# Kernel tuning notes

Measured on AMD Instinct MI355X. Metric: run time of the kernel, lower is better.

## Reference

```python
import jax, jax.numpy as jnp
import numpy as np

B, S, H, F, E, K = 4, 2048, 512, 2048, 8, 2


def setup_inputs() -> dict:
    key = jax.random.key(0)
    ks = jax.random.split(key, 6)
    s_h = 1.0 / np.sqrt(H)
    s_f = 1.0 / np.sqrt(F)
    return {
        "x": jax.random.normal(ks[0], (B, S, H), dtype=jnp.float32),
        "router_w": jax.random.uniform(ks[1], (E, H), jnp.float32, -s_h, s_h),
        "fc1_w": jax.random.uniform(ks[2], (E, F, H), jnp.float32, -s_h, s_h),
        "fc1_b": jax.random.uniform(ks[3], (E, F), jnp.float32, -s_h, s_h),
        "fc2_w": jax.random.uniform(ks[4], (E, H, F), jnp.float32, -s_f, s_f),
        "fc2_b": jax.random.uniform(ks[5], (E, H), jnp.float32, -s_f, s_f),
    }


def reference(x, router_w, fc1_w, fc1_b, fc2_w, fc2_b):
    # Router: Linear (no bias), softmax over experts, top-k, renormalize.
    logits = jnp.einsum("bsh,eh->bse", x, router_w)           # [B,S,E]
    probs = jax.nn.softmax(logits, axis=-1)                    # [B,S,E]
    topk_p, topk_i = jax.lax.top_k(probs, K)                   # [B,S,K]
    topk_p = topk_p / (jnp.sum(topk_p, axis=-1, keepdims=True) + 1e-9)

    # Original loop runs every expert FFN on all tokens and masks;
    # mathematically identical: dense per-expert FFN, then gather+combine.
    h1 = jnp.einsum("bsh,efh->bsef", x, fc1_w) + fc1_b         # [B,S,E,F]
    a = jax.nn.gelu(h1, approximate=False)                     # exact erf GELU (torch nn.GELU default)
    y = jnp.einsum("bsef,ehf->bseh", a, fc2_w) + fc2_b         # [B,S,E,H]

    sel = jnp.take_along_axis(y, topk_i[..., None], axis=2)    # [B,S,K,H]
    output = jnp.sum(topk_p[..., None] * sel, axis=2)          # [B,S,H]
    return output, probs, topk_i
```

## Files before the change

kernel.cpp:

```cpp
#include <hip/hip_runtime.h>

#define T_TOKENS 8192
#define HD 512
#define FD 2048
#define NE 8
#define CAP 8192
#define CSTRIDE 32

typedef __attribute__((ext_vector_type(8))) short short8;
typedef __attribute__((ext_vector_type(4))) float f32x4;

__device__ __forceinline__ ushort f2bf(float f) {
  union { float f; unsigned u; } v; v.f = f;
  unsigned u = v.u;
  return (ushort)((u + 0x7fffu + ((u >> 16) & 1u)) >> 16);
}

__device__ __forceinline__ void gld16(const ushort* g, ushort* l) {
  __builtin_amdgcn_global_load_lds(
      (const __attribute__((address_space(1))) void*)g,
      (__attribute__((address_space(3))) void*)l, 16, 0, 0);
}

__global__ void cvt_bf16_3(const float4* __restrict__ s0, ushort4* __restrict__ d0, int c0,
                           const float4* __restrict__ s1, ushort4* __restrict__ d1, int c1,
                           const float4* __restrict__ s2, ushort4* __restrict__ d2, int c2) {
  int i = blockIdx.x * blockDim.x + threadIdx.x;
  int st = gridDim.x * blockDim.x;
  int nt = c0 + c1 + c2;
  for (; i < nt; i += st) {
    const float4* s; ushort4* d; int j = i;
    if (j < c0) { s = s0; d = d0; }
    else if ((j -= c0) < c1) { s = s1; d = d1; }
    else { j -= c1; s = s2; d = d2; }
    float4 v = s[j];
    ushort4 o;
    o.x = f2bf(v.x); o.y = f2bf(v.y); o.z = f2bf(v.z); o.w = f2bf(v.w);
    d[j] = o;
  }
}

#define TPW 16
__global__ void router_kernel(const float* __restrict__ x, const float* __restrict__ rw,
                              float* __restrict__ probs_out, float* __restrict__ topk_out,
                              int* __restrict__ counts, int* __restrict__ bucket_tok,
                              float* __restrict__ bucket_w, int4* __restrict__ tok_info) {
  __shared__ int lcnt[NE];
  __shared__ int lbase[NE];
  __shared__ int ls_e0[64], ls_e1[64], ls_s0[64], ls_s1[64];
  __shared__ float ls_w0[64], ls_w1[64];

  int wave = threadIdx.x >> 6, lane = threadIdx.x & 63;
  if (threadIdx.x < NE) lcnt[threadIdx.x] = 0;
  __syncthreads();

  int tbase = blockIdx.x * 64;
  for (int it = 0; it < TPW; it++) {
    int lt = wave * TPW + it;
    int t = tbase + lt;
    float acc[NE];
#pragma unroll
    for (int e = 0; e < NE; e++) acc[e] = 0.f;
    const float* xr = x + (size_t)t * HD;
    for (int c = 0; c < HD; c += 64) {
      float xv = xr[c + lane];
#pragma unroll
      for (int e = 0; e < NE; e++) acc[e] += xv * rw[e * HD + c + lane];
    }
#pragma unroll
    for (int e = 0; e < NE; e++) {
#pragma unroll
      for (int s = 32; s > 0; s >>= 1) acc[e] += __shfl_xor(acc[e], s, 64);
    }
    if (lane == 0) {
      float m = acc[0];
#pragma unroll
      for (int e = 1; e < NE; e++) m = fmaxf(m, acc[e]);
      float p[NE], s = 0.f;
#pragma unroll
      for (int e = 0; e < NE; e++) { p[e] = expf(acc[e] - m); s += p[e]; }
      float inv = 1.f / s;
#pragma unroll
      for (int e = 0; e < NE; e++) { p[e] *= inv; probs_out[(size_t)t * NE + e] = p[e]; }
      int i0 = 0;
#pragma unroll
      for (int e = 1; e < NE; e++) if (p[e] > p[i0]) i0 = e;
      int i1 = (i0 == 0) ? 1 : 0;
#pragma unroll
      for (int e = 0; e < NE; e++) if (e != i0 && p[e] > p[i1]) i1 = e;
      float r = 1.f / (p[i0] + p[i1] + 1e-9f);
      topk_out[(size_t)t * 2 + 0] = (float)i0;
      topk_out[(size_t)t * 2 + 1] = (float)i1;
      ls_e0[lt] = i0; ls_e1[lt] = i1;
      ls_w0[lt] = p[i0] * r; ls_w1[lt] = p[i1] * r;
      ls_s0[lt] = atomicAdd(&lcnt[i0], 1);
      ls_s1[lt] = atomicAdd(&lcnt[i1], 1);
    }
  }
  __syncthreads();
  if (threadIdx.x < NE)
    lbase[threadIdx.x] = atomicAdd(&counts[threadIdx.x * CSTRIDE], lcnt[threadIdx.x]);
  __syncthreads();
  if (threadIdx.x < 64) {
    int lt = threadIdx.x, t = tbase + lt;
    int e0 = ls_e0[lt], e1 = ls_e1[lt];
    int g0 = lbase[e0] + ls_s0[lt];
    int g1 = lbase[e1] + ls_s1[lt];
    bucket_tok[e0 * CAP + g0] = t; bucket_w[e0 * CAP + g0] = ls_w0[lt];
    bucket_tok[e1 * CAP + g1] = t; bucket_w[e1 * CAP + g1] = ls_w1[lt];
    tok_info[t] = make_int4(e0, e1, g0, g1);
  }
}

__global__ void scan_kernel(const int* __restrict__ counts, int* __restrict__ offsets) {
  if (threadIdx.x == 0) {
    int o = 0;
#pragma unroll
    for (int e = 0; e < NE; e++) { offsets[e] = o; o += counts[e * CSTRIDE]; }
  }
}


__device__ __forceinline__ short8 ldsr32(const ushort* base, int row, int q) {
  int a = row * 64 + q * 16;
  a ^= ((row >> 1) & 3) << 4;
  return *(const short8*)((const char*)base + a);
}

#define VMC(N) asm volatile("s_waitcnt vmcnt(" #N ")" ::: "memory")
#define SB0 __builtin_amdgcn_sched_barrier(0)

#define STG3(KT, SB_) do { \
    ushort* _la = bufA + (SB_) * TU + tid * 8; \
    ushort* _lb = bufB + (SB_) * TU + tid * 8; \
    gld16(aS0 + (KT) * 32, _la); gld16(aS1 + (KT) * 32, _la + 2048); \
    gld16(bS0 + (KT) * 32, _lb); gld16(bS1 + (KT) * 32, _lb + 2048); \
  } while (0)

#define CMP3(RB_) do { \
    const ushort* _As = bufA + (RB_) * TU; \
    const ushort* _Bs = bufB + (RB_) * TU; \
    short8 af[4], bfr[4]; \
    _Pragma("unroll") for (int mi = 0; mi < 4; ++mi) \
      af[mi] = ldsr32(_As, wm * 64 + mi * 16 + l16, q); \
    _Pragma("unroll") for (int nj = 0; nj < 4; ++nj) \
      bfr[nj] = ldsr32(_Bs, wn * 64 + nj * 16 + l16, q); \
    asm volatile("s_waitcnt lgkmcnt(0)" ::: "memory"); SB0; \
    __builtin_amdgcn_s_setprio(1); \
    _Pragma("unroll") for (int mi = 0; mi < 4; ++mi) \
      _Pragma("unroll") for (int nj = 0; nj < 4; ++nj) \
        acc[mi][nj] = __builtin_amdgcn_mfma_f32_16x16x32_bf16(af[mi], bfr[nj], acc[mi][nj], 0, 0, 0); \
    __builtin_amdgcn_s_setprio(0); \
  } while (0)

template <bool IS_FC1>
__global__ __launch_bounds__(256, 3)
void ffn_gemm_p3(const ushort* __restrict__ Ab, const ushort* __restrict__ Bw,
                 const float* __restrict__ bias, const int* __restrict__ counts,
                 const int* __restrict__ offsets, const int* __restrict__ bucket_tok,
                 const float* __restrict__ bucket_w, ushort* __restrict__ Aout,
                 float* __restrict__ Yout, int KD, int ND) {
  constexpr int TU = 128 * 32;

  int e = blockIdx.z;
  int cnt = counts[e * CSTRIDE];
  int m0 = blockIdx.y * 128;
  if (m0 >= cnt) return;
  int n0 = blockIdx.x * 128;
  int off = offsets[e];

  extern __shared__ ushort smem[];
  ushort* bufA = smem;
  ushort* bufB = smem + 3 * TU;

  int tid = threadIdx.x;
  int lid = tid & 63, w = tid >> 6;
  int wm = w >> 1, wn = w & 1;
  int q = lid >> 4, l16 = lid & 15;
  int r0 = tid >> 2;
  int colElem = (((tid & 3) ^ ((r0 >> 1) & 3)) << 3);

  const ushort *aS0, *aS1, *bS0, *bS1;
  {
    int rA0 = min(m0 + r0, cnt - 1);
    int rA1 = min(m0 + 64 + r0, cnt - 1);
    int t0 = IS_FC1 ? bucket_tok[e * CAP + rA0] : (off + rA0);
    int t1 = IS_FC1 ? bucket_tok[e * CAP + rA1] : (off + rA1);
    aS0 = Ab + (size_t)t0 * KD + colElem;
    aS1 = Ab + (size_t)t1 * KD + colElem;
    bS0 = Bw + ((size_t)e * ND + n0 + r0) * KD + colElem;
    bS1 = Bw + ((size_t)e * ND + n0 + 64 + r0) * KD + colElem;
  }

  f32x4 acc[4][4] = {};
  int nk = KD >> 5;

  STG3(0, 0); STG3(1, 1);
  int rb = 0, sb = 2;
  for (int k = 0; k < nk - 2; ++k) {
    STG3(k + 2, sb); SB0;
    VMC(8); SB0;
    __builtin_amdgcn_s_barrier(); SB0;
    CMP3(rb);
    SB0; __builtin_amdgcn_s_barrier();
    rb = (rb == 2) ? 0 : rb + 1;
    sb = (sb == 2) ? 0 : sb + 1;
  }
  VMC(4); SB0; __builtin_amdgcn_s_barrier(); SB0;
  CMP3(rb); SB0; __builtin_amdgcn_s_barrier();
  rb = (rb == 2) ? 0 : rb + 1;
  VMC(0); SB0; __builtin_amdgcn_s_barrier(); SB0;
  CMP3(rb); SB0; __builtin_amdgcn_s_barrier();

  float bcol[4];
#pragma unroll
  for (int j = 0; j < 4; ++j)
    bcol[j] = bias[(size_t)e * ND + n0 + wn * 64 + j * 16 + l16];

  if (IS_FC1) {
    ushort* Ct = smem;
#pragma unroll
    for (int i = 0; i < 4; i++) {
      __syncthreads();
#pragma unroll
      for (int j = 0; j < 4; j++)
#pragma unroll
        for (int r = 0; r < 4; r++) {
          float v = acc[i][j][r] + bcol[j];
          float g = 0.5f * v * (1.0f + erff(v * 0.70710678118654752f));
          Ct[(wm * 16 + q * 4 + r) * 136 + wn * 64 + j * 16 + l16] = f2bf(g);
        }
      __syncthreads();
#pragma unroll
      for (int u = 0; u < 2; u++) {
        int c = tid + u * 256;
        int ml = c >> 4, cc = c & 15;
        int gm = m0 + (ml >> 4) * 64 + i * 16 + (ml & 15);
        if (gm < cnt)
          *(uint4*)&Aout[(size_t)(off + gm) * ND + n0 + cc * 8] =
              *(const uint4*)&Ct[ml * 136 + cc * 8];
      }
    }
  } else {
    float* Cf = (float*)smem;
#pragma unroll
    for (int i = 0; i < 4; i++) {
      __syncthreads();
#pragma unroll
      for (int r = 0; r < 4; r++) {
        int gm = m0 + wm * 64 + i * 16 + q * 4 + r;
        float wgt = bucket_w[e * CAP + min(gm, cnt - 1)];
#pragma unroll
        for (int j = 0; j < 4; j++)
          Cf[(wm * 16 + q * 4 + r) * 132 + wn * 64 + j * 16 + l16] = wgt * (acc[i][j][r] + bcol[j]);
      }
      __syncthreads();
#pragma unroll
      for (int u = 0; u < 4; u++) {
        int c = tid + u * 256;
        int ml = c >> 5, cc = c & 31;
        int gm = m0 + (ml >> 4) * 64 + i * 16 + (ml & 15);
        if (gm < cnt)
          *(float4*)&Yout[(size_t)(off + gm) * ND + n0 + cc * 4] =
              *(const float4*)&Cf[ml * 132 + cc * 4];
      }
    }
  }
}

__global__ void combine_kernel(const float4* __restrict__ Y, const int4* __restrict__ tok_info,
                               const int* __restrict__ offsets, float4* __restrict__ out) {
  int t = blockIdx.x;
  int4 ti = tok_info[t];
  int g0 = offsets[ti.x] + ti.z;
  int g1 = offsets[ti.y] + ti.w;
  int i = threadIdx.x;
  float4 a = Y[(size_t)g0 * (HD / 4) + i];
  float4 b = Y[(size_t)g1 * (HD / 4) + i];
  out[(size_t)t * (HD / 4) + i] = make_float4(a.x + b.x, a.y + b.y, a.z + b.z, a.w + b.w);
}

extern "C" void kernel_launch(void* const* d_in, const int* in_sizes, int n_in,
                              void* d_out, int out_size, void* d_ws, size_t ws_size,
                              hipStream_t stream) {
  const float* x    = (const float*)d_in[0];
  const float* rw   = (const float*)d_in[1];
  const float* fc1w = (const float*)d_in[2];
  const float* fc1b = (const float*)d_in[3];
  const float* fc2w = (const float*)d_in[4];
  const float* fc2b = (const float*)d_in[5];

  float* out   = (float*)d_out;
  float* probs = out + (size_t)T_TOKENS * HD;
  float* topk  = probs + (size_t)T_TOKENS * NE;

  static bool attr_done = false;
  if (!attr_done) {
    (void)hipFuncSetAttribute((const void*)&ffn_gemm_p3<true>,
                              hipFuncAttributeMaxDynamicSharedMemorySize, 49152);
    (void)hipFuncSetAttribute((const void*)&ffn_gemm_p3<false>,
                              hipFuncAttributeMaxDynamicSharedMemorySize, 49152);
    attr_done = true;
  }

  char* p = (char*)d_ws;
  auto carve = [&](size_t bytes) { char* r = p; p += (bytes + 255) & ~(size_t)255; return r; };
  int*    counts     = (int*)carve(NE * CSTRIDE * sizeof(int));
  int*    offsets    = (int*)carve(NE * sizeof(int));
  int*    bucket_tok = (int*)carve((size_t)NE * CAP * sizeof(int));
  float*  bucket_w   = (float*)carve((size_t)NE * CAP * sizeof(float));
  int4*   tok_info   = (int4*)carve((size_t)T_TOKENS * sizeof(int4));
  ushort* xb   = (ushort*)carve((size_t)T_TOKENS * HD * 2);
  ushort* w1b  = (ushort*)carve((size_t)NE * FD * HD * 2);
  ushort* w2b  = (ushort*)carve((size_t)NE * HD * FD * 2);
  ushort* Abuf = (ushort*)carve((size_t)T_TOKENS * 2 * FD * 2);
  float*  Y    = (float*)carve((size_t)T_TOKENS * 2 * HD * 4);

  hipMemsetAsync(counts, 0, NE * CSTRIDE * sizeof(int), stream);
  cvt_bf16_3<<<4096, 256, 0, stream>>>(
      (const float4*)x,    (ushort4*)xb,  T_TOKENS * HD / 4,
      (const float4*)fc1w, (ushort4*)w1b, NE * FD * HD / 4,
      (const float4*)fc2w, (ushort4*)w2b, NE * HD * FD / 4);
  router_kernel<<<T_TOKENS / 64, 256, 0, stream>>>(x, rw, probs, topk, counts, bucket_tok,
                                                   bucket_w, tok_info);
  scan_kernel<<<1, 64, 0, stream>>>(counts, offsets);

  ffn_gemm_p3<true><<<dim3(FD / 128, CAP / 128, NE), 256, 49152, stream>>>(
      xb, w1b, fc1b, counts, offsets, bucket_tok, bucket_w, Abuf, nullptr, HD, FD);
  ffn_gemm_p3<false><<<dim3(HD / 128, CAP / 128, NE), 256, 49152, stream>>>(
      Abuf, w2b, fc2b, counts, offsets, bucket_tok, bucket_w, nullptr, Y, FD, HD);

  combine_kernel<<<T_TOKENS, 128, 0, stream>>>((const float4*)Y, tok_info, offsets, (float4*)out);
}
```

Baseline: 314.3 us.

## Fuse x bf16 cast into router, template GEMM dims, use fast GELU

```diff
diff --git a/kernel.cpp b/kernel.cpp
--- a/kernel.cpp
+++ b/kernel.cpp
@@ -22,17 +22,28 @@
       (__attribute__((address_space(3))) void*)l, 16, 0, 0);
 }
 
-__global__ void cvt_bf16_3(const float4* __restrict__ s0, ushort4* __restrict__ d0, int c0,
-                           const float4* __restrict__ s1, ushort4* __restrict__ d1, int c1,
-                           const float4* __restrict__ s2, ushort4* __restrict__ d2, int c2) {
+__device__ __forceinline__ float gelu_fast(float v) {
+  float u = v * 0.70710678118654752f;
+  float x = fabsf(u);
+  float d = __builtin_fmaf(0.3275911f, x, 1.0f);
+  float t;
+  asm("v_rcp_f32 %0, %1" : "=v"(t) : "v"(d));
+  float y = t * (0.254829592f + t * (-0.284496736f +
+            t * (1.421413741f + t * (-1.453152027f + t * 1.061405429f))));
+  float erfabs = __builtin_fmaf(-y, __expf(-x * x), 1.0f);
+  float erfv = copysignf(erfabs, u);
+  return 0.5f * v * (1.0f + erfv);
+}
+
+__global__ void cvt_bf16_2(const float4* __restrict__ s0, ushort4* __restrict__ d0, int c0,
+                           const float4* __restrict__ s1, ushort4* __restrict__ d1, int c1) {
   int i = blockIdx.x * blockDim.x + threadIdx.x;
   int st = gridDim.x * blockDim.x;
-  int nt = c0 + c1 + c2;
+  int nt = c0 + c1;
   for (; i < nt; i += st) {
     const float4* s; ushort4* d; int j = i;
     if (j < c0) { s = s0; d = d0; }
-    else if ((j -= c0) < c1) { s = s1; d = d1; }
-    else { j -= c1; s = s2; d = d2; }
+    else { j -= c0; s = s1; d = d1; }
     float4 v = s[j];
     ushort4 o;
     o.x = f2bf(v.x); o.y = f2bf(v.y); o.z = f2bf(v.z); o.w = f2bf(v.w);
@@ -44,7 +55,8 @@
 __global__ void router_kernel(const float* __restrict__ x, const float* __restrict__ rw,
                               float* __restrict__ probs_out, float* __restrict__ topk_out,
                               int* __restrict__ counts, int* __restrict__ bucket_tok,
-                              float* __restrict__ bucket_w, int4* __restrict__ tok_info) {
+                              float* __restrict__ bucket_w, int4* __restrict__ tok_info,
+                              ushort* __restrict__ xb) {
   __shared__ int lcnt[NE];
   __shared__ int lbase[NE];
   __shared__ int ls_e0[64], ls_e1[64], ls_s0[64], ls_s1[64];
@@ -62,8 +74,10 @@
 #pragma unroll
     for (int e = 0; e < NE; e++) acc[e] = 0.f;
     const float* xr = x + (size_t)t * HD;
+    ushort* xbr = xb + (size_t)t * HD;
     for (int c = 0; c < HD; c += 64) {
       float xv = xr[c + lane];
+      xbr[c + lane] = f2bf(xv);
 #pragma unroll
       for (int e = 0; e < NE; e++) acc[e] += xv * rw[e * HD + c + lane];
     }
@@ -153,14 +167,16 @@
     __builtin_amdgcn_s_setprio(0); \
   } while (0)
 
-template <bool IS_FC1>
+template <bool IS_FC1, int KD_, int ND_>
 __global__ __launch_bounds__(256, 3)
 void ffn_gemm_p3(const ushort* __restrict__ Ab, const ushort* __restrict__ Bw,
                  const float* __restrict__ bias, const int* __restrict__ counts,
                  const int* __restrict__ offsets, const int* __restrict__ bucket_tok,
                  const float* __restrict__ bucket_w, ushort* __restrict__ Aout,
-                 float* __restrict__ Yout, int KD, int ND) {
+                 float* __restrict__ Yout) {
   constexpr int TU = 128 * 32;
+  constexpr int NK = KD_ >> 5;
+  static_assert(NK >= 3, "pipeline needs >= 3 K-steps");
 
   int e = blockIdx.z;
   int cnt = counts[e * CSTRIDE];
@@ -186,36 +202,32 @@
     int rA1 = min(m0 + 64 + r0, cnt - 1);
     int t0 = IS_FC1 ? bucket_tok[e * CAP + rA0] : (off + rA0);
     int t1 = IS_FC1 ? bucket_tok[e * CAP + rA1] : (off + rA1);
-    aS0 = Ab + (size_t)t0 * KD + colElem;
-    aS1 = Ab + (size_t)t1 * KD + colElem;
-    bS0 = Bw + ((size_t)e * ND + n0 + r0) * KD + colElem;
-    bS1 = Bw + ((size_t)e * ND + n0 + 64 + r0) * KD + colElem;
+    aS0 = Ab + (size_t)t0 * KD_ + colElem;
+    aS1 = Ab + (size_t)t1 * KD_ + colElem;
+    bS0 = Bw + ((size_t)e * ND_ + n0 + r0) * KD_ + colElem;
+    bS1 = Bw + ((size_t)e * ND_ + n0 + 64 + r0) * KD_ + colElem;
   }
 
   f32x4 acc[4][4] = {};
-  int nk = KD >> 5;
 
   STG3(0, 0); STG3(1, 1);
-  int rb = 0, sb = 2;
-  for (int k = 0; k < nk - 2; ++k) {
-    STG3(k + 2, sb); SB0;
+#pragma unroll
+  for (int k = 0; k < NK - 2; ++k) {
+    STG3(k + 2, (k + 2) % 3); SB0;
     VMC(8); SB0;
     __builtin_amdgcn_s_barrier(); SB0;
-    CMP3(rb);
+    CMP3(k % 3);
     SB0; __builtin_amdgcn_s_barrier();
-    rb = (rb == 2) ? 0 : rb + 1;
-    sb = (sb == 2) ? 0 : sb + 1;
   }
   VMC(4); SB0; __builtin_amdgcn_s_barrier(); SB0;
-  CMP3(rb); SB0; __builtin_amdgcn_s_barrier();
-  rb = (rb == 2) ? 0 : rb + 1;
+  CMP3((NK - 2) % 3); SB0; __builtin_amdgcn_s_barrier();
   VMC(0); SB0; __builtin_amdgcn_s_barrier(); SB0;
-  CMP3(rb); SB0; __builtin_amdgcn_s_barrier();
+  CMP3((NK - 1) % 3); SB0; __builtin_amdgcn_s_barrier();
 
   float bcol[4];
 #pragma unroll
   for (int j = 0; j < 4; ++j)
-    bcol[j] = bias[(size_t)e * ND + n0 + wn * 64 + j * 16 + l16];
+    bcol[j] = bias[(size_t)e * ND_ + n0 + wn * 64 + j * 16 + l16];
 
   if (IS_FC1) {
     ushort* Ct = smem;
@@ -227,8 +239,7 @@
 #pragma unroll
         for (int r = 0; r < 4; r++) {
           float v = acc[i][j][r] + bcol[j];
-          float g = 0.5f * v * (1.0f + erff(v * 0.70710678118654752f));
-          Ct[(wm * 16 + q * 4 + r) * 136 + wn * 64 + j * 16 + l16] = f2bf(g);
+          Ct[(wm * 16 + q * 4 + r) * 136 + wn * 64 + j * 16 + l16] = f2bf(gelu_fast(v));
         }
       __syncthreads();
 #pragma unroll
@@ -237,7 +248,7 @@
         int ml = c >> 4, cc = c & 15;
         int gm = m0 + (ml >> 4) * 64 + i * 16 + (ml & 15);
         if (gm < cnt)
-          *(uint4*)&Aout[(size_t)(off + gm) * ND + n0 + cc * 8] =
+          *(uint4*)&Aout[(size_t)(off + gm) * ND_ + n0 + cc * 8] =
               *(const uint4*)&Ct[ml * 136 + cc * 8];
       }
     }
@@ -261,7 +272,7 @@
         int ml = c >> 5, cc = c & 31;
         int gm = m0 + (ml >> 4) * 64 + i * 16 + (ml & 15);
         if (gm < cnt)
-          *(float4*)&Yout[(size_t)(off + gm) * ND + n0 + cc * 4] =
+          *(float4*)&Yout[(size_t)(off + gm) * ND_ + n0 + cc * 4] =
               *(const float4*)&Cf[ml * 132 + cc * 4];
       }
     }
@@ -296,9 +307,9 @@
 
   static bool attr_done = false;
   if (!attr_done) {
-    (void)hipFuncSetAttribute((const void*)&ffn_gemm_p3<true>,
+    (void)hipFuncSetAttribute((const void*)&ffn_gemm_p3<true, HD, FD>,
                               hipFuncAttributeMaxDynamicSharedMemorySize, 49152);
-    (void)hipFuncSetAttribute((const void*)&ffn_gemm_p3<false>,
+    (void)hipFuncSetAttribute((const void*)&ffn_gemm_p3<false, FD, HD>,
                               hipFuncAttributeMaxDynamicSharedMemorySize, 49152);
     attr_done = true;
   }
@@ -317,18 +328,17 @@
   float*  Y    = (float*)carve((size_t)T_TOKENS * 2 * HD * 4);
 
   hipMemsetAsync(counts, 0, NE * CSTRIDE * sizeof(int), stream);
-  cvt_bf16_3<<<4096, 256, 0, stream>>>(
-      (const float4*)x,    (ushort4*)xb,  T_TOKENS * HD / 4,
+  cvt_bf16_2<<<4096, 256, 0, stream>>>(
       (const float4*)fc1w, (ushort4*)w1b, NE * FD * HD / 4,
       (const float4*)fc2w, (ushort4*)w2b, NE * HD * FD / 4);
   router_kernel<<<T_TOKENS / 64, 256, 0, stream>>>(x, rw, probs, topk, counts, bucket_tok,
-                                                   bucket_w, tok_info);
+                                                   bucket_w, tok_info, xb);
   scan_kernel<<<1, 64, 0, stream>>>(counts, offsets);
 
-  ffn_gemm_p3<true><<<dim3(FD / 128, CAP / 128, NE), 256, 49152, stream>>>(
-      xb, w1b, fc1b, counts, offsets, bucket_tok, bucket_w, Abuf, nullptr, HD, FD);
-  ffn_gemm_p3<false><<<dim3(HD / 128, CAP / 128, NE), 256, 49152, stream>>>(
-      Abuf, w2b, fc2b, counts, offsets, bucket_tok, bucket_w, nullptr, Y, FD, HD);
+  ffn_gemm_p3<true, HD, FD><<<dim3(FD / 128, CAP / 128, NE), 256, 49152, stream>>>(
+      xb, w1b, fc1b, counts, offsets, bucket_tok, bucket_w, Abuf, nullptr);
+  ffn_gemm_p3<false, FD, HD><<<dim3(HD / 128, CAP / 128, NE), 256, 49152, stream>>>(
+      Abuf, w2b, fc2b, counts, offsets, bucket_tok, bucket_w, nullptr, Y);
 
   combine_kernel<<<T_TOKENS, 128, 0, stream>>>((const float4*)Y, tok_info, offsets, (float4*)out);
 }
```

Measured after the change: 298.1 us. -5.1%, faster.
